# Kernel tuning notes

Measured on AMD Instinct MI355X. Metric: run time of the kernel, lower is better.

## Reference

```python
import jax, jax.numpy as jnp
import numpy as np

B, N, D = 4, 4096, 512
K = 16384          # codebook size
NUM_Q = 2          # residual quantizers (shared codebook)


def setup_inputs() -> dict:
    key = jax.random.key(0)
    ks = jax.random.split(key, 6)
    s = 1.0 / np.sqrt(D)
    return {
        "x": jax.random.normal(ks[0], (B, N, D), dtype=jnp.float32),
        "enc_w": jax.random.normal(ks[1], (D, D), dtype=jnp.float32) * s,
        "enc_b": jnp.zeros((D,), dtype=jnp.float32),
        "codebook": jax.random.normal(ks[2], (K, D), dtype=jnp.float32),
        "dec_w": jax.random.normal(ks[3], (D, D), dtype=jnp.float32) * s,
        "dec_b": jnp.zeros((D,), dtype=jnp.float32),
    }


def _residual_vq(z, codebook):
    # z: [B, N, D] -> flatten tokens
    flat = z.reshape(-1, z.shape[-1])          # [T, D]
    c_sq = jnp.sum(codebook * codebook, axis=-1)  # [K]
    q_sum = jnp.zeros_like(flat)
    residual = flat
    for _ in range(NUM_Q):
        # argmin of ||r - c||^2 == argmin of (||c||^2 - 2 r.c); skip ||r||^2
        dists = c_sq[None, :] - 2.0 * (residual @ codebook.T)  # [T, K]
        idx = jnp.argmin(dists, axis=-1)                       # [T]
        q = codebook[idx]                                      # gather [T, D]
        q_sum = q_sum + q
        residual = residual - q
    return q_sum.reshape(z.shape)


def reference(x, enc_w, enc_b, codebook, dec_w, dec_b):
    z = x @ enc_w.T + enc_b                     # encoder Linear(512 -> 512)
    q = _residual_vq(z, codebook)               # sum of per-stage code vectors
    z_tilde = z + jax.lax.stop_gradient(q - z)  # straight-through estimator
    x_recon = z_tilde @ dec_w.T + dec_b         # decoder Linear(512 -> 512)
    return x_recon
```

## Files before the change

kernel.cpp:

```cpp
#include <hip/hip_runtime.h>
#include <stdint.h>

constexpr int TT = 16384;
constexpr int DD = 512;
constexpr int KK = 16384;
constexpr int TOPK = 8;

typedef __bf16 bf16x8 __attribute__((ext_vector_type(8)));
typedef __bf16 bf16x4 __attribute__((ext_vector_type(4)));
typedef float f32x4 __attribute__((ext_vector_type(4)));

typedef const __attribute__((address_space(1))) void* gas_ptr;
typedef __attribute__((address_space(3))) void* las_ptr;

__device__ __forceinline__ unsigned long long pack_di(float d, int idx) {
    uint32_t u = __float_as_uint(d);
    u = (u & 0x80000000u) ? ~u : (u | 0x80000000u);
    return ((unsigned long long)u << 32) | (uint32_t)idx;
}

__device__ __forceinline__ unsigned long long umin64(unsigned long long a,
                                                     unsigned long long b) {
    return a < b ? a : b;
}
__device__ __forceinline__ uint32_t umin32(uint32_t a, uint32_t b) { return a < b ? a : b; }
__device__ __forceinline__ uint32_t umax32(uint32_t a, uint32_t b) { return a > b ? a : b; }

__device__ __forceinline__ uint32_t sortable(float d) {
    uint32_t u = __float_as_uint(d);
    return u ^ ((uint32_t)((int32_t)u >> 31) | 0x80000000u);
}

template<int MODE>
__global__ __launch_bounds__(256)
void gemm_mfma(const float* __restrict__ A, const float* __restrict__ A2,
               const float* __restrict__ W, const float* __restrict__ bias,
               float* __restrict__ out0, float* __restrict__ out1,
               __bf16* __restrict__ out2)
{
    __shared__ __bf16 Ah[128 * 64], Al[128 * 64];
    __shared__ __bf16 Bh[128 * 64], Bl[128 * 64];
    const int tid = threadIdx.x;
    const int lane = tid & 63;
    const int w = tid >> 6;
    const int row0 = blockIdx.y * 128;
    const int col0 = blockIdx.x * 128;

    f32x4 acc[2][8] = {};

    const int sr = tid >> 4;
    const int scol = (tid & 15) * 4;
    const int lcol = (((scol >> 3) ^ (sr & 7)) << 3) + (scol & 7);

    int a_off[2], b_off[8];
    #pragma unroll
    for (int mi = 0; mi < 2; ++mi) {
        const int ar = w * 32 + mi * 16 + (lane & 15);
        a_off[mi] = ar * 64 + (((lane >> 4) ^ (ar & 7)) << 3);
    }
    #pragma unroll
    for (int ni = 0; ni < 8; ++ni) {
        const int br = ni * 16 + (lane & 15);
        b_off[ni] = br * 64 + (((lane >> 4) ^ (br & 7)) << 3);
    }

    for (int kb = 0; kb < 512; kb += 64) {
        __syncthreads();
        #pragma unroll
        for (int i = 0; i < 8; ++i) {
            const int r = i * 16 + sr;
            float4 v = *(const float4*)(A + (size_t)(row0 + r) * 512 + kb + scol);
            if (MODE == 1) {
                const float4 u = *(const float4*)(A2 + (size_t)(row0 + r) * 512 + kb + scol);
                v.x -= u.x; v.y -= u.y; v.z -= u.z; v.w -= u.w;
            }
            bf16x4 hv, lv;
            hv[0] = (__bf16)v.x; hv[1] = (__bf16)v.y; hv[2] = (__bf16)v.z; hv[3] = (__bf16)v.w;
            lv[0] = (__bf16)(v.x - (float)hv[0]); lv[1] = (__bf16)(v.y - (float)hv[1]);
            lv[2] = (__bf16)(v.z - (float)hv[2]); lv[3] = (__bf16)(v.w - (float)hv[3]);
            *(bf16x4*)(Ah + r * 64 + lcol) = hv;
            *(bf16x4*)(Al + r * 64 + lcol) = lv;

            const float4 x = *(const float4*)(W + (size_t)(col0 + r) * 512 + kb + scol);
            bf16x4 hw, lw;
            hw[0] = (__bf16)x.x; hw[1] = (__bf16)x.y; hw[2] = (__bf16)x.z; hw[3] = (__bf16)x.w;
            lw[0] = (__bf16)(x.x - (float)hw[0]); lw[1] = (__bf16)(x.y - (float)hw[1]);
            lw[2] = (__bf16)(x.z - (float)hw[2]); lw[3] = (__bf16)(x.w - (float)hw[3]);
            *(bf16x4*)(Bh + r * 64 + lcol) = hw;
            *(bf16x4*)(Bl + r * 64 + lcol) = lw;
        }
        __syncthreads();
        #pragma unroll
        for (int s = 0; s < 2; ++s) {
            const int sx = s * 32;
            bf16x8 ah[2], al[2];
            #pragma unroll
            for (int mi = 0; mi < 2; ++mi) {
                ah[mi] = *(const bf16x8*)(Ah + (a_off[mi] ^ sx));
                al[mi] = *(const bf16x8*)(Al + (a_off[mi] ^ sx));
            }
            #pragma unroll
            for (int ni = 0; ni < 8; ++ni) {
                const bf16x8 bh = *(const bf16x8*)(Bh + (b_off[ni] ^ sx));
                const bf16x8 bl = *(const bf16x8*)(Bl + (b_off[ni] ^ sx));
                #pragma unroll
                for (int mi = 0; mi < 2; ++mi) {
                    acc[mi][ni] = __builtin_amdgcn_mfma_f32_16x16x32_bf16(ah[mi], bh, acc[mi][ni], 0, 0, 0);
                    acc[mi][ni] = __builtin_amdgcn_mfma_f32_16x16x32_bf16(ah[mi], bl, acc[mi][ni], 0, 0, 0);
                    acc[mi][ni] = __builtin_amdgcn_mfma_f32_16x16x32_bf16(al[mi], bh, acc[mi][ni], 0, 0, 0);
                }
            }
        }
    }

    #pragma unroll
    for (int mi = 0; mi < 2; ++mi) {
        #pragma unroll
        for (int reg = 0; reg < 4; ++reg) {
            const int row = row0 + w * 32 + mi * 16 + (lane >> 4) * 4 + reg;
            #pragma unroll
            for (int ni = 0; ni < 8; ++ni) {
                const int col = col0 + ni * 16 + (lane & 15);
                const float o = acc[mi][ni][reg] + bias[col];
                out0[(size_t)row * 512 + col] = o;
                if (MODE == 0) {
                    out1[(size_t)row * 512 + col] = o;
                    out2[(size_t)row * 512 + col] = (__bf16)o;
                }
            }
        }
    }
}

__global__ __launch_bounds__(512, 2)
void dist_approx8(const __bf16* __restrict__ Rh,
                  const __bf16* __restrict__ Ch,
                  const float* __restrict__ csq,
                  uint32_t* __restrict__ winners)
{
    __shared__ __bf16 As[2][256 * 64];
    __shared__ __bf16 Bs[2][256 * 64];

    const int tid  = threadIdx.x;
    const int lane = tid & 63;
    const int w    = tid >> 6;
    const int wm   = w >> 2;
    const int wn   = w & 3;

    const int wg   = (blockIdx.x & 7) * 512 + (blockIdx.x >> 3);
    const int col0 = (wg & 63) << 8;
    const int row0 = (wg >> 6) << 8;

    f32x4 acc[8][4] = {};

    const int s_r = tid >> 3;
    const int s_c = (tid & 7) ^ (s_r & 7);
    const __bf16* aS = Rh + (size_t)(row0 + s_r) * 512 + s_c * 8;
    const __bf16* bS = Ch + (size_t)(col0 + s_r) * 512 + s_c * 8;
    __bf16* const lA0 = &As[0][0]; __bf16* const lA1 = &As[1][0];
    __bf16* const lB0 = &Bs[0][0]; __bf16* const lB1 = &Bs[1][0];

#define STAGE(SRC, UOFF, DST)                                                      \
    {                                                                              \
        __builtin_amdgcn_global_load_lds((gas_ptr)((SRC) + (UOFF)),                \
                                         (las_ptr)((DST) + w * 8 * 64), 16, 0, 0); \
        __builtin_amdgcn_global_load_lds((gas_ptr)((SRC) + (UOFF) + 64 * 512),     \
                                         (las_ptr)((DST) + (64 + w * 8) * 64), 16, 0, 0); \
    }

    int aoff[8], boff[4];
    #pragma unroll
    for (int mi = 0; mi < 8; ++mi) {
        const int r = wm * 128 + mi * 16 + (lane & 15);
        aoff[mi] = r * 64 + (((lane >> 4) ^ (r & 7)) << 3);
    }
    #pragma unroll
    for (int ni = 0; ni < 4; ++ni) {
        const int r = wn * 64 + ni * 16 + (lane & 15);
        boff[ni] = r * 64 + (((lane >> 4) ^ (r & 7)) << 3);
    }

#define BAR __builtin_amdgcn_s_barrier()
#define LGKM0 { asm volatile("s_waitcnt lgkmcnt(0)" ::: "memory"); \
                __builtin_amdgcn_sched_barrier(0); }
#define MFMA_QUAD(AF, A0, BV)                                                  \
    {                                                                          \
        __builtin_amdgcn_s_setprio(1);                                         \
        _Pragma("unroll")                                                      \
        for (int mi = 0; mi < 4; ++mi) {                                       \
            _Pragma("unroll")                                                  \
            for (int ni = 0; ni < 4; ++ni)                                     \
                acc[(A0) + mi][ni] = __builtin_amdgcn_mfma_f32_16x16x32_bf16(  \
                    (AF)[(A0) + mi], (BV)[ni], acc[(A0) + mi][ni], 0, 0, 0);   \
        }                                                                      \
        __builtin_amdgcn_s_setprio(0);                                         \
    }

    STAGE(aS, 0,              lA0);
    STAGE(aS, 128 * 512,      lA0 + 128 * 64);
    STAGE(bS, 0,              lB0);
    STAGE(bS, 128 * 512,      lB0 + 128 * 64);
    STAGE(aS, 64,             lA1);
    STAGE(aS, 128 * 512 + 64, lA1 + 128 * 64);
    asm volatile("s_waitcnt vmcnt(4)" ::: "memory");
    BAR;

    bf16x8 a0[8], a1[8], b0[4], b1[4];

    for (int it = 0; it < 4; ++it) {
        const bool more = it < 3;
        const int kb1 = (2 * it + 1) * 64;
        const int kb2 = (2 * it + 2) * 64;
        const int kb3 = (2 * it + 3) * 64;

        #pragma unroll
        for (int mi = 0; mi < 8; ++mi) a0[mi] = *(const bf16x8*)(lA0 + aoff[mi]);
        #pragma unroll
        for (int ni = 0; ni < 4; ++ni) b0[ni] = *(const bf16x8*)(lB0 + boff[ni]);
        STAGE(bS, kb1, lB1);
        BAR; LGKM0;
        MFMA_QUAD(a0, 0, b0);
        BAR;

        #pragma unroll
        for (int mi = 0; mi < 8; ++mi) a1[mi] = *(const bf16x8*)(lA0 + (aoff[mi] ^ 32));
        STAGE(bS, 128 * 512 + kb1, lB1 + 128 * 64);
        BAR; LGKM0;
        MFMA_QUAD(a0, 4, b0);
        BAR;

        #pragma unroll
        for (int ni = 0; ni < 4; ++ni) b1[ni] = *(const bf16x8*)(lB0 + (boff[ni] ^ 32));
        if (more) STAGE(aS, kb2, lA0);
        BAR; LGKM0;
        MFMA_QUAD(a1, 0, b1);
        BAR;

        if (more) STAGE(aS, 128 * 512 + kb2, lA0 + 128 * 64);
        BAR;
        MFMA_QUAD(a1, 4, b1);
        if (more) { asm volatile("s_waitcnt vmcnt(4)" ::: "memory"); }
        else      { asm volatile("s_waitcnt vmcnt(0)" ::: "memory"); }
        BAR;

        #pragma unroll
        for (int mi = 0; mi < 8; ++mi) a0[mi] = *(const bf16x8*)(lA1 + aoff[mi]);
        #pragma unroll
        for (int ni = 0; ni < 4; ++ni) b0[ni] = *(const bf16x8*)(lB1 + boff[ni]);
        if (more) STAGE(bS, kb2, lB0);
        BAR; LGKM0;
        MFMA_QUAD(a0, 0, b0);
        BAR;

        #pragma unroll
        for (int mi = 0; mi < 8; ++mi) a1[mi] = *(const bf16x8*)(lA1 + (aoff[mi] ^ 32));
        if (more) STAGE(bS, 128 * 512 + kb2, lB0 + 128 * 64);
        BAR; LGKM0;
        MFMA_QUAD(a0, 4, b0);
        BAR;

        #pragma unroll
        for (int ni = 0; ni < 4; ++ni) b1[ni] = *(const bf16x8*)(lB1 + (boff[ni] ^ 32));
        if (more) STAGE(aS, kb3, lA1);
        BAR; LGKM0;
        MFMA_QUAD(a1, 0, b1);
        BAR;

        if (more) STAGE(aS, 128 * 512 + kb3, lA1 + 128 * 64);
        BAR;
        MFMA_QUAD(a1, 4, b1);
        if (more) { asm volatile("s_waitcnt vmcnt(4)" ::: "memory"); }
        BAR;
    }

    float csv[4];
    #pragma unroll
    for (int ni = 0; ni < 4; ++ni)
        csv[ni] = csq[col0 + wn * 64 + ni * 16 + (lane & 15)];

    const int tile = (col0 >> 6) + wn;
    #pragma unroll
    for (int mi = 0; mi < 8; ++mi) {
        #pragma unroll
        for (int reg = 0; reg < 4; ++reg) {
            uint32_t b = 0xFFFFFFFFu, s = 0xFFFFFFFFu;
            #pragma unroll
            for (int ni = 0; ni < 4; ++ni) {
                const float d = fmaf(-2.0f, acc[mi][ni][reg], csv[ni]);
                const uint32_t key = (sortable(d) & 0xFFFFFFC0u)
                                   | (uint32_t)(ni * 16 + (lane & 15));
                const uint32_t nb = umin32(b, key);
                s = umin32(s, umax32(b, key));
                b = nb;
            }
            #pragma unroll
            for (int m = 1; m < 16; m <<= 1) {
                const uint32_t ob = __shfl_xor((int)b, m, 16);
                const uint32_t os = __shfl_xor((int)s, m, 16);
                const uint32_t nb = umin32(b, ob);
                s = umin32(umin32(s, os), umax32(b, ob));
                b = nb;
            }
            if ((lane & 15) == 0) {
                const int row = row0 + wm * 128 + mi * 16 + (lane >> 4) * 4 + reg;
                uint2 v; v.x = b; v.y = s;
                *(uint2*)(winners + (size_t)row * 512 + tile * 2) = v;
            }
        }
    }
#undef STAGE
#undef BAR
#undef LGKM0
#undef MFMA_QUAD
}

__global__ __launch_bounds__(256)
void select_rescore(const uint32_t* __restrict__ winners,
                    const float* __restrict__ CB, const float* __restrict__ csq,
                    float* __restrict__ R, __bf16* __restrict__ R16)
{
    const int w = threadIdx.x >> 6;
    const int lane = threadIdx.x & 63;
    const int token = blockIdx.x * 4 + w;

    const uint32_t* wt = winners + (size_t)token * 512;
    uint4 q0 = *(const uint4*)(wt + lane * 8);
    uint4 q1 = *(const uint4*)(wt + lane * 8 + 4);
    uint32_t k32[8] = {q0.x, q0.y, q0.z, q0.w, q1.x, q1.y, q1.z, q1.w};

    unsigned long long v[8];
    #pragma unroll
    for (int j = 0; j < 8; ++j) {
        const int gcol = ((lane * 8 + j) >> 1) * 64 + (int)(k32[j] & 63u);
        v[j] = ((unsigned long long)k32[j] << 32) | (uint32_t)gcol;
    }

    unsigned long long cand[TOPK];
    #pragma unroll
    for (int t = 0; t < TOPK; ++t) {
        unsigned long long mm = v[0];
        #pragma unroll
        for (int j = 1; j < 8; ++j) mm = umin64(mm, v[j]);
        #pragma unroll
        for (int m = 1; m < 64; m <<= 1)
            mm = umin64(mm, __shfl_xor(mm, m, 64));
        cand[t] = mm;
        #pragma unroll
        for (int j = 0; j < 8; ++j) if (v[j] == mm) v[j] = ~0ull;
    }

    float4 r0 = *(const float4*)(R + (size_t)token * 512 + lane * 8);
    float4 r1 = *(const float4*)(R + (size_t)token * 512 + lane * 8 + 4);

    unsigned long long best = ~0ull;
    #pragma unroll
    for (int t = 0; t < TOPK; ++t) {
        const int col = (int)(cand[t] & 0xFFFFFFFFull);
        const float4 c0 = *(const float4*)(CB + (size_t)col * 512 + lane * 8);
        const float4 c1 = *(const float4*)(CB + (size_t)col * 512 + lane * 8 + 4);
        float dot = r0.x * c0.x;
        dot = fmaf(r0.y, c0.y, dot); dot = fmaf(r0.z, c0.z, dot);
        dot = fmaf(r0.w, c0.w, dot); dot = fmaf(r1.x, c1.x, dot);
        dot = fmaf(r1.y, c1.y, dot); dot = fmaf(r1.z, c1.z, dot);
        dot = fmaf(r1.w, c1.w, dot);
        #pragma unroll
        for (int m = 1; m < 64; m <<= 1) dot += __shfl_xor(dot, m, 64);
        const float d = fmaf(-2.0f, dot, csq[col]);
        best = umin64(best, pack_di(d, col));
    }

    const int bcol = (int)(best & 0xFFFFFFFFull);
    const float4 c0 = *(const float4*)(CB + (size_t)bcol * 512 + lane * 8);
    const float4 c1 = *(const float4*)(CB + (size_t)bcol * 512 + lane * 8 + 4);
    r0.x -= c0.x; r0.y -= c0.y; r0.z -= c0.z; r0.w -= c0.w;
    r1.x -= c1.x; r1.y -= c1.y; r1.z -= c1.z; r1.w -= c1.w;
    *(float4*)(R + (size_t)token * 512 + lane * 8) = r0;
    *(float4*)(R + (size_t)token * 512 + lane * 8 + 4) = r1;
    bf16x8 h;
    h[0] = (__bf16)r0.x; h[1] = (__bf16)r0.y; h[2] = (__bf16)r0.z; h[3] = (__bf16)r0.w;
    h[4] = (__bf16)r1.x; h[5] = (__bf16)r1.y; h[6] = (__bf16)r1.z; h[7] = (__bf16)r1.w;
    *(bf16x8*)(R16 + (size_t)token * 512 + lane * 8) = h;
}

__global__ __launch_bounds__(256)
void prep_cb(const float* __restrict__ CB, float* __restrict__ c_sq,
             __bf16* __restrict__ cb16)
{
    const int wave = threadIdx.x >> 6;
    const int lane = threadIdx.x & 63;
    const int row = blockIdx.x * 4 + wave;
    const float* p = CB + (size_t)row * DD + lane * 8;
    const float4 a = *(const float4*)p;
    const float4 b = *(const float4*)(p + 4);
    bf16x8 h;
    h[0] = (__bf16)a.x; h[1] = (__bf16)a.y; h[2] = (__bf16)a.z; h[3] = (__bf16)a.w;
    h[4] = (__bf16)b.x; h[5] = (__bf16)b.y; h[6] = (__bf16)b.z; h[7] = (__bf16)b.w;
    *(bf16x8*)(cb16 + (size_t)row * DD + lane * 8) = h;
    float s = a.x*a.x + a.y*a.y + a.z*a.z + a.w*a.w
            + b.x*b.x + b.y*b.y + b.z*b.z + b.w*b.w;
    #pragma unroll
    for (int m = 1; m < 64; m <<= 1) s += __shfl_xor(s, m, 64);
    if (lane == 0) c_sq[row] = s;
}

extern "C" void kernel_launch(void* const* d_in, const int* in_sizes, int n_in,
                              void* d_out, int out_size, void* d_ws, size_t ws_size,
                              hipStream_t stream)
{
    const float* x    = (const float*)d_in[0];
    const float* encw = (const float*)d_in[1];
    const float* encb = (const float*)d_in[2];
    const float* cb   = (const float*)d_in[3];
    const float* decw = (const float*)d_in[4];
    const float* decb = (const float*)d_in[5];
    float* out = (float*)d_out;

    float* z    = (float*)d_ws;
    float* r    = z + (size_t)TT * DD;
    __bf16* cb16 = (__bf16*)(r + (size_t)TT * DD);
    __bf16* r16  = cb16 + (size_t)KK * DD;
    float* csq  = (float*)(r16 + (size_t)TT * DD);
    uint32_t* winners = (uint32_t*)d_out;

    const dim3 blk(256);

    gemm_mfma<0><<<dim3(DD / 128, TT / 128), blk, 0, stream>>>(
        x, nullptr, encw, encb, z, r, r16);

    prep_cb<<<dim3(KK / 4), blk, 0, stream>>>(cb, csq, cb16);

    for (int s = 0; s < 2; ++s) {
        dist_approx8<<<dim3((TT / 256) * (KK / 256)), dim3(512), 0, stream>>>(
            r16, cb16, csq, winners);
        select_rescore<<<dim3(TT / 4), blk, 0, stream>>>(winners, cb, csq, r, r16);
    }

    gemm_mfma<1><<<dim3(DD / 128, TT / 128), blk, 0, stream>>>(
        z, r, decw, decb, out, nullptr, nullptr);
}
```

Measured before the change: 1.129 ms.

## Chain four row tiles per distance workgroup for persistent-style streaming

Each dist_approx8 workgroup now handles four consecutive 256-row token tiles against one 256-column codebook tile. It keeps the pipeline running across tile boundaries and emits top-2 winners after every fourth iteration. The grid shrinks by four, and the block-to-XCD mapping is reworked so each XCD covers a band of codebook columns. This is meant to cut per-workgroup prologue and epilogue cost and to improve L2 reuse of codebook tiles. In exchange, B tiles are reloaded per chained tile and the epilogue now stalls the pipeline mid-stream.

```diff
diff --git a/kernel.cpp b/kernel.cpp
--- a/kernel.cpp
+++ b/kernel.cpp
@@ -132,6 +132,9 @@
     }
 }
 
+constexpr int CHAIN = 4;
+constexpr size_t TILE_A = 256 * 512;
+
 __global__ __launch_bounds__(512, 2)
 void dist_approx8(const __bf16* __restrict__ Rh,
                   const __bf16* __restrict__ Ch,
@@ -147,18 +150,24 @@
     const int wm   = w >> 2;
     const int wn   = w & 3;
 
-    const int wg   = (blockIdx.x & 7) * 512 + (blockIdx.x >> 3);
-    const int col0 = (wg & 63) << 8;
-    const int row0 = (wg >> 6) << 8;
+    const int b    = blockIdx.x;
+    const int xcd  = b & 7;
+    const int i    = b >> 3;
+    const int ct   = xcd * 8 + (i & 7);
+    const int tg   = i >> 3;
+    const int col0 = ct << 8;
+    const int rowb = tg << 10;
 
     f32x4 acc[8][4] = {};
 
     const int s_r = tid >> 3;
     const int s_c = (tid & 7) ^ (s_r & 7);
-    const __bf16* aS = Rh + (size_t)(row0 + s_r) * 512 + s_c * 8;
+    const __bf16* aS = Rh + (size_t)(rowb + s_r) * 512 + s_c * 8;
     const __bf16* bS = Ch + (size_t)(col0 + s_r) * 512 + s_c * 8;
     __bf16* const lA0 = &As[0][0]; __bf16* const lA1 = &As[1][0];
     __bf16* const lB0 = &Bs[0][0]; __bf16* const lB1 = &Bs[1][0];
+
+#define AOFF(q) ((size_t)((q) >> 3) * TILE_A + (size_t)((q) & 7) * 64)
 
 #define STAGE(SRC, UOFF, DST)                                                      \
     {                                                                              \
@@ -196,47 +205,54 @@
         __builtin_amdgcn_s_setprio(0);                                         \
     }
 
-    STAGE(aS, 0,              lA0);
-    STAGE(aS, 128 * 512,      lA0 + 128 * 64);
-    STAGE(bS, 0,              lB0);
-    STAGE(bS, 128 * 512,      lB0 + 128 * 64);
-    STAGE(aS, 64,             lA1);
-    STAGE(aS, 128 * 512 + 64, lA1 + 128 * 64);
+    float csv[4];
+    #pragma unroll
+    for (int ni = 0; ni < 4; ++ni)
+        csv[ni] = csq[col0 + wn * 64 + ni * 16 + (lane & 15)];
+    const int gt = (col0 >> 6) + wn;
+
+    STAGE(aS, AOFF(0),             lA0);
+    STAGE(aS, AOFF(0) + 128 * 512, lA0 + 128 * 64);
+    STAGE(bS, 0,                   lB0);
+    STAGE(bS, 128 * 512,           lB0 + 128 * 64);
+    STAGE(aS, AOFF(1),             lA1);
+    STAGE(aS, AOFF(1) + 128 * 512, lA1 + 128 * 64);
     asm volatile("s_waitcnt vmcnt(4)" ::: "memory");
     BAR;
 
     bf16x8 a0[8], a1[8], b0[4], b1[4];
 
-    for (int it = 0; it < 4; ++it) {
-        const bool more = it < 3;
-        const int kb1 = (2 * it + 1) * 64;
-        const int kb2 = (2 * it + 2) * 64;
-        const int kb3 = (2 * it + 3) * 64;
+    for (int it = 0; it < 4 * CHAIN; ++it) {
+        const bool more = it < 4 * CHAIN - 1;
+        const size_t oB1 = (size_t)((2 * it + 1) & 7) * 64;
+        const size_t oA2 = AOFF(2 * it + 2);
+        const size_t oB2 = (size_t)((2 * it + 2) & 7) * 64;
+        const size_t oA3 = AOFF(2 * it + 3);
 
         #pragma unroll
         for (int mi = 0; mi < 8; ++mi) a0[mi] = *(const bf16x8*)(lA0 + aoff[mi]);
         #pragma unroll
         for (int ni = 0; ni < 4; ++ni) b0[ni] = *(const bf16x8*)(lB0 + boff[ni]);
-        STAGE(bS, kb1, lB1);
+        STAGE(bS, oB1, lB1);
         BAR; LGKM0;
         MFMA_QUAD(a0, 0, b0);
         BAR;
 
         #pragma unroll
         for (int mi = 0; mi < 8; ++mi) a1[mi] = *(const bf16x8*)(lA0 + (aoff[mi] ^ 32));
-        STAGE(bS, 128 * 512 + kb1, lB1 + 128 * 64);
+        STAGE(bS, 128 * 512 + oB1, lB1 + 128 * 64);
         BAR; LGKM0;
         MFMA_QUAD(a0, 4, b0);
         BAR;
 
         #pragma unroll
         for (int ni = 0; ni < 4; ++ni) b1[ni] = *(const bf16x8*)(lB0 + (boff[ni] ^ 32));
-        if (more) STAGE(aS, kb2, lA0);
+        if (more) STAGE(aS, oA2, lA0);
         BAR; LGKM0;
         MFMA_QUAD(a1, 0, b1);
         BAR;
 
-        if (more) STAGE(aS, 128 * 512 + kb2, lA0 + 128 * 64);
+        if (more) STAGE(aS, oA2 + 128 * 512, lA0 + 128 * 64);
         BAR;
         MFMA_QUAD(a1, 4, b1);
         if (more) { asm volatile("s_waitcnt vmcnt(4)" ::: "memory"); }
@@ -247,68 +263,71 @@
         for (int mi = 0; mi < 8; ++mi) a0[mi] = *(const bf16x8*)(lA1 + aoff[mi]);
         #pragma unroll
         for (int ni = 0; ni < 4; ++ni) b0[ni] = *(const bf16x8*)(lB1 + boff[ni]);
-        if (more) STAGE(bS, kb2, lB0);
+        if (more) STAGE(bS, oB2, lB0);
         BAR; LGKM0;
         MFMA_QUAD(a0, 0, b0);
         BAR;
 
         #pragma unroll
         for (int mi = 0; mi < 8; ++mi) a1[mi] = *(const bf16x8*)(lA1 + (aoff[mi] ^ 32));
-        if (more) STAGE(bS, 128 * 512 + kb2, lB0 + 128 * 64);
+        if (more) STAGE(bS, 128 * 512 + oB2, lB0 + 128 * 64);
         BAR; LGKM0;
         MFMA_QUAD(a0, 4, b0);
         BAR;
 
         #pragma unroll
         for (int ni = 0; ni < 4; ++ni) b1[ni] = *(const bf16x8*)(lB1 + (boff[ni] ^ 32));
-        if (more) STAGE(aS, kb3, lA1);
+        if (more) STAGE(aS, oA3, lA1);
         BAR; LGKM0;
         MFMA_QUAD(a1, 0, b1);
         BAR;
 
-        if (more) STAGE(aS, 128 * 512 + kb3, lA1 + 128 * 64);
+        if (more) STAGE(aS, oA3 + 128 * 512, lA1 + 128 * 64);
         BAR;
         MFMA_QUAD(a1, 4, b1);
         if (more) { asm volatile("s_waitcnt vmcnt(4)" ::: "memory"); }
         BAR;
-    }
-
-    float csv[4];
-    #pragma unroll
-    for (int ni = 0; ni < 4; ++ni)
-        csv[ni] = csq[col0 + wn * 64 + ni * 16 + (lane & 15)];
-
-    const int tile = (col0 >> 6) + wn;
-    #pragma unroll
-    for (int mi = 0; mi < 8; ++mi) {
-        #pragma unroll
-        for (int reg = 0; reg < 4; ++reg) {
-            uint32_t b = 0xFFFFFFFFu, s = 0xFFFFFFFFu;
+
+        if ((it & 3) == 3) {
+            const int r0t = rowb + (it >> 2) * 256;
             #pragma unroll
-            for (int ni = 0; ni < 4; ++ni) {
-                const float d = fmaf(-2.0f, acc[mi][ni][reg], csv[ni]);
-                const uint32_t key = (sortable(d) & 0xFFFFFFC0u)
-                                   | (uint32_t)(ni * 16 + (lane & 15));
-                const uint32_t nb = umin32(b, key);
-                s = umin32(s, umax32(b, key));
-                b = nb;
+            for (int mi = 0; mi < 8; ++mi) {
+                #pragma unroll
+                for (int reg = 0; reg < 4; ++reg) {
+                    uint32_t bk = 0xFFFFFFFFu, sk = 0xFFFFFFFFu;
+                    #pragma unroll
+                    for (int ni = 0; ni < 4; ++ni) {
+                        const float d = fmaf(-2.0f, acc[mi][ni][reg], csv[ni]);
+                        const uint32_t key = (sortable(d) & 0xFFFFFFC0u)
+                                           | (uint32_t)(ni * 16 + (lane & 15));
+                        const uint32_t nb = umin32(bk, key);
+                        sk = umin32(sk, umax32(bk, key));
+                        bk = nb;
+                    }
+                    #pragma unroll
+                    for (int m = 1; m < 16; m <<= 1) {
+                        const uint32_t ob = __shfl_xor((int)bk, m, 16);
+                        const uint32_t os = __shfl_xor((int)sk, m, 16);
+                        const uint32_t nb = umin32(bk, ob);
+                        sk = umin32(umin32(sk, os), umax32(bk, ob));
+                        bk = nb;
+                    }
+                    if ((lane & 15) == 0) {
+                        const int row = r0t + wm * 128 + mi * 16 + (lane >> 4) * 4 + reg;
+                        uint2 v; v.x = bk; v.y = sk;
+                        *(uint2*)(winners + (size_t)row * 512 + gt * 2) = v;
+                    }
+                }
             }
             #pragma unroll
-            for (int m = 1; m < 16; m <<= 1) {
-                const uint32_t ob = __shfl_xor((int)b, m, 16);
-                const uint32_t os = __shfl_xor((int)s, m, 16);
-                const uint32_t nb = umin32(b, ob);
-                s = umin32(umin32(s, os), umax32(b, ob));
-                b = nb;
-            }
-            if ((lane & 15) == 0) {
-                const int row = row0 + wm * 128 + mi * 16 + (lane >> 4) * 4 + reg;
-                uint2 v; v.x = b; v.y = s;
-                *(uint2*)(winners + (size_t)row * 512 + tile * 2) = v;
-            }
+            for (int mi = 0; mi < 8; ++mi)
+                #pragma unroll
+                for (int ni = 0; ni < 4; ++ni)
+                    acc[mi][ni] = (f32x4){0.f, 0.f, 0.f, 0.f};
         }
     }
 #undef STAGE
+#undef AOFF
 #undef BAR
 #undef LGKM0
 #undef MFMA_QUAD
@@ -430,7 +449,7 @@
     prep_cb<<<dim3(KK / 4), blk, 0, stream>>>(cb, csq, cb16);
 
     for (int s = 0; s < 2; ++s) {
-        dist_approx8<<<dim3((TT / 256) * (KK / 256)), dim3(512), 0, stream>>>(
+        dist_approx8<<<dim3((KK / 256) * (TT / 256 / CHAIN)), dim3(512), 0, stream>>>(
             r16, cb16, csq, winners);
         select_rescore<<<dim3(TT / 4), blk, 0, stream>>>(winners, cb, csq, r, r16);
     }
```

Result: faster. 1.047 ms (-7.3%).
